# Kernel tuning notes

Hardware: AMD Instinct MI355X
Metric: run time of the kernel (lower is better)

## Reference

```python
import jax, jax.numpy as jnp
import numpy as np

B, T, D = 2, 2048, 1024
HEADS, UNITS = 16, 64
OUT_DIM = 1024
_LARGE_BIAS = 10000.0


def _uniform(key, shape, fan_in, fan_out):
    limit = np.sqrt(6.0 / (fan_in + fan_out))
    return jax.random.uniform(key, shape, jnp.float32, -limit, limit)


def setup_inputs() -> dict:
    key = jax.random.key(0)
    kx, kq, kk, kv, ko = jax.random.split(key, 5)
    x = jax.random.normal(kx, (B, T, D), jnp.float32)
    mask = jnp.ones((B, T), jnp.int32)
    Wq = _uniform(kq, (D, HEADS * UNITS), D, UNITS)
    Wk = _uniform(kk, (D, HEADS * UNITS), D, UNITS)
    Wv = _uniform(kv, (D, HEADS * UNITS), D, UNITS)
    Wo = _uniform(ko, (HEADS * UNITS, OUT_DIM), HEADS * UNITS, OUT_DIM)
    return {"x": x, "mask": mask, "Wq": Wq, "Wk": Wk, "Wv": Wv, "Wo": Wo}


def reference(x, mask, Wq, Wk, Wv, Wo):
    m = mask.astype(x.dtype)                      # [B, T]
    x = x * m[:, :, None]                         # zero padded positions
    b, t, _ = x.shape
    # projections, split heads: [B, T, H, U]
    q = (x @ Wq).reshape(b, t, HEADS, UNITS)
    k = (x @ Wk).reshape(b, t, HEADS, UNITS)
    v = (x @ Wv).reshape(b, t, HEADS, UNITS)
    # logits[b,h,i,j] = sum_u q[b,i,h,u] k[b,j,h,u]
    logits = jnp.einsum('bihu,bjhu->bhij', q, k) / np.sqrt(UNITS).astype(x.dtype)
    # causal (forward) mask: subtract large bias above the diagonal
    causal = jnp.triu(jnp.full((t, t), _LARGE_BIAS, x.dtype), k=1)
    logits = logits - causal
    # padding mask on key axis
    logits = logits - ((1.0 - m) * _LARGE_BIAS)[:, None, None, :]
    weights = jax.nn.softmax(logits, axis=-1)     # [B, H, T, T]
    attended = jnp.einsum('bhij,bjhu->bihu', weights, v)
    attended = attended.reshape(b, t, HEADS * UNITS)
    return attended @ Wo                          # [B, T, OUT_DIM]
```

## Files before the change

### kernel.cpp

```cpp
#include <hip/hip_runtime.h>
#include <stdint.h>
#include <stddef.h>

#define B_ 2
#define T_ 2048
#define D_ 1024
#define H_ 16
#define U_ 64
#define M_ (B_ * T_)
#define N_ (H_ * U_)

typedef __attribute__((ext_vector_type(4))) float f32x4;
typedef __attribute__((ext_vector_type(8))) short s16x8;
typedef __attribute__((ext_vector_type(8))) __bf16 b16x8;

static_assert(sizeof(s16x8) == 16, "frag size");

__device__ __forceinline__ unsigned short f2bf(float f) {
  unsigned int u = __float_as_uint(f);
  u += 0x7FFFu + ((u >> 16) & 1u);
  return (unsigned short)(u >> 16);
}

template <typename V>
__device__ __forceinline__ auto mfma16_impl(V a, V b, f32x4 c, int)
    -> decltype(__builtin_amdgcn_mfma_f32_16x16x32_bf16(a, b, c, 0, 0, 0)) {
  return __builtin_amdgcn_mfma_f32_16x16x32_bf16(a, b, c, 0, 0, 0);
}
template <typename V>
__device__ __forceinline__ f32x4 mfma16_impl(V a, V b, f32x4 c, long) {
  return __builtin_amdgcn_mfma_f32_16x16x32_bf16(
      __builtin_bit_cast(b16x8, a), __builtin_bit_cast(b16x8, b), c, 0, 0, 0);
}
__device__ __forceinline__ f32x4 mfma16(s16x8 a, s16x8 b, f32x4 c) {
  return mfma16_impl(a, b, c, 0);
}

__device__ __forceinline__ void gld16(const unsigned short* g, unsigned short* l) {
  __builtin_amdgcn_global_load_lds(
      (const __attribute__((address_space(1))) void*)g,
      (__attribute__((address_space(3))) void*)l, 16, 0, 0);
}

__global__ void wtrans_kernel(const float* __restrict__ w0, const float* __restrict__ w1,
                              const float* __restrict__ w2, const float* __restrict__ w3,
                              unsigned short* __restrict__ o0, unsigned short* __restrict__ o1,
                              unsigned short* __restrict__ o2, unsigned short* __restrict__ o3) {
  __shared__ float tile[64][65];
  const float* w;
  unsigned short* o;
  switch (blockIdx.z) {
    case 0: w = w0; o = o0; break;
    case 1: w = w1; o = o1; break;
    case 2: w = w2; o = o2; break;
    default: w = w3; o = o3; break;
  }
  const int kb = blockIdx.y * 64, nb = blockIdx.x * 64;
  const int tid = threadIdx.x;
  const int r0 = tid >> 6, c = tid & 63;
#pragma unroll
  for (int i = 0; i < 16; i++) {
    int r = i * 4 + r0;
    tile[r][c] = w[(size_t)(kb + r) * 1024 + nb + c];
  }
  __syncthreads();
#pragma unroll
  for (int i = 0; i < 16; i++) {
    int r = i * 4 + r0;
    o[(size_t)(nb + r) * 1024 + kb + c] = f2bf(tile[c][r]);
  }
}

__global__ void xmask_kernel(const float* __restrict__ x, const int* __restrict__ mask,
                             unsigned short* __restrict__ xb) {
  const int idx = (blockIdx.x * 256 + threadIdx.x) * 4;
  const int row = idx >> 10;
  const float m = (float)mask[row];
  float4 v = *(const float4*)(x + idx);
  ushort4 o;
  o.x = f2bf(v.x * m);
  o.y = f2bf(v.y * m);
  o.z = f2bf(v.z * m);
  o.w = f2bf(v.w * m);
  *(ushort4*)(xb + idx) = o;
}

template <int MODE>
__device__ __forceinline__ void gemm97_body(const unsigned short* __restrict__ A,
                                            const unsigned short* __restrict__ Bt,
                                            void* __restrict__ Cout) {
  constexpr int Kd = 1024, Nd = 1024;
  __shared__ unsigned short la[128 * 32];
  __shared__ unsigned short lb[128 * 32];
  const int tid = threadIdx.x;
  const int lane = tid & 63;
  const int w = tid >> 6;
  const int mb = blockIdx.y * 128, nb = blockIdx.x * 128;
  const int wm = (w >> 1) * 64, wn = (w & 1) * 64;
  const int lr = lane & 15, lg = lane >> 4;
  const int srow = w * 16 + (lane >> 2);
  const int scol = (lane & 3) * 8;
  const unsigned short* gA = A + (size_t)(mb + srow) * Kd + scol;
  const unsigned short* gB = Bt + (size_t)(nb + srow) * Kd + scol;
  unsigned short* lA = la + srow * 32 + scol;
  unsigned short* lB = lb + srow * 32 + scol;

  f32x4 acc[4][4] = {};

  for (int kt = 0; kt < Kd; kt += 32) {
    gld16(gA + kt, lA);
    gld16(gA + kt + (size_t)64 * Kd, lA + 64 * 32);
    gld16(gB + kt, lB);
    gld16(gB + kt + (size_t)64 * Kd, lB + 64 * 32);
    __syncthreads();
    s16x8 af[4], bfr[4];
#pragma unroll
    for (int i = 0; i < 4; i++)
      af[i] = *(const s16x8*)(la + (wm + i * 16 + lr) * 32 + lg * 8);
#pragma unroll
    for (int j = 0; j < 4; j++)
      bfr[j] = *(const s16x8*)(lb + (wn + j * 16 + lr) * 32 + lg * 8);
#pragma unroll
    for (int i = 0; i < 4; i++)
#pragma unroll
      for (int j = 0; j < 4; j++)
        acc[i][j] = mfma16(af[i], bfr[j], acc[i][j]);
    __syncthreads();
  }

#pragma unroll
  for (int i = 0; i < 4; i++)
#pragma unroll
    for (int j = 0; j < 4; j++) {
      const int col = nb + wn + j * 16 + lr;
      const int rowb = mb + wm + i * 16 + lg * 4;
      if (MODE == 1) {
        float* C = (float*)Cout;
#pragma unroll
        for (int r = 0; r < 4; r++) C[(size_t)(rowb + r) * Nd + col] = acc[i][j][r];
      } else if (MODE == 0) {
        unsigned short* C = (unsigned short*)Cout;
#pragma unroll
        for (int r = 0; r < 4; r++) C[(size_t)(rowb + r) * Nd + col] = f2bf(acc[i][j][r]);
      } else {
        unsigned short* C = (unsigned short*)Cout;
        const size_t vrow = ((size_t)(rowb >> 11) * 16 + (col >> 6)) * 64 + (col & 63);
        ushort4 o;
#pragma unroll
        for (int r = 0; r < 4; r++) ((unsigned short*)&o)[r] = f2bf(acc[i][j][r]);
        *(ushort4*)(C + vrow * T_ + (rowb & 2047)) = o;
      }
    }
}

__global__ __launch_bounds__(256) void gemm_qkv(const unsigned short* __restrict__ A,
                                                const unsigned short* __restrict__ wq,
                                                const unsigned short* __restrict__ wk,
                                                const unsigned short* __restrict__ wv,
                                                unsigned short* __restrict__ cq,
                                                unsigned short* __restrict__ ck,
                                                unsigned short* __restrict__ vt) {
  if (blockIdx.z == 0) {
    gemm97_body<0>(A, wq, cq);
  } else if (blockIdx.z == 1) {
    gemm97_body<0>(A, wk, ck);
  } else {
    gemm97_body<2>(A, wv, vt);
  }
}

__global__ __launch_bounds__(256) void gemm_out(const unsigned short* __restrict__ A,
                                                const unsigned short* __restrict__ woT,
                                                float* __restrict__ C) {
  gemm97_body<1>(A, woT, C);
}

__global__ __launch_bounds__(64) void attn12_kernel(const unsigned short* __restrict__ Q,
                                                    const unsigned short* __restrict__ K,
                                                    const unsigned short* __restrict__ Vt,
                                                    const int* __restrict__ mask,
                                                    unsigned short* __restrict__ att) {
  __shared__ unsigned short pbuf[32 * 64];
  const int lane = threadIdx.x & 63;
  const int li = lane & 15, lg = lane >> 4;
  const int bh = blockIdx.x & 31;
  const int b = bh >> 4, h = bh & 15;
  const int qg = 63 - (blockIdx.x >> 5);
  const int q0 = qg * 32;

  const float CS = 0.125f * 1.44269504089f;
  const float PB = 10000.0f * 1.44269504089f;
  const float THR = 8.0f;

  s16x8 qf[2][2];
#pragma unroll
  for (int f = 0; f < 2; f++) {
    const unsigned short* qrow = Q + ((size_t)(b * T_) + q0 + f * 16 + li) * 1024 + h * 64;
    qf[f][0] = *(const s16x8*)(qrow + lg * 8);
    qf[f][1] = *(const s16x8*)(qrow + 32 + lg * 8);
  }

  const unsigned short* Kb = K + (size_t)(b * T_) * 1024 + h * 64;
  const unsigned short* Vtb = Vt + (size_t)bh * 64 * T_;
  const int* mk = mask + b * T_;

  const int iq0 = q0 + li, iq1 = q0 + 16 + li;

  float mrun[2] = {-1e30f, -1e30f};
  float lpart[2] = {0.f, 0.f};
  f32x4 acc[4][2] = {};

  const int xr = (li & 3) << 5;
  char* pbb = (char*)pbuf;

  const int ntiles = (q0 + 95) >> 6;
  for (int t = 0; t < ntiles; t++) {
    const int jb = t * 64;
    const bool diag = (jb + 64 > q0);

    int4 mv[4];
#pragma unroll
    for (int jf = 0; jf < 4; jf++)
      mv[jf] = *(const int4*)(mk + jb + jf * 16 + lg * 4);

    f32x4 s[4][2] = {};
#pragma unroll
    for (int jf = 0; jf < 4; jf++) {
      const unsigned short* kr = Kb + (size_t)(jb + jf * 16 + li) * 1024 + lg * 8;
      s16x8 ka = *(const s16x8*)kr;
      s16x8 kc = *(const s16x8*)(kr + 32);
      s[jf][0] = mfma16(ka, qf[0][0], s[jf][0]);
      s[jf][0] = mfma16(kc, qf[0][1], s[jf][0]);
      s[jf][1] = mfma16(ka, qf[1][0], s[jf][1]);
      s[jf][1] = mfma16(kc, qf[1][1], s[jf][1]);
    }

    s16x8 vf[4][2];
#pragma unroll
    for (int uf = 0; uf < 4; uf++) {
      const unsigned short* vr = Vtb + (size_t)(uf * 16 + li) * T_ + jb + lg * 8;
      vf[uf][0] = *(const s16x8*)vr;
      vf[uf][1] = *(const s16x8*)(vr + 32);
    }

    float bias[4][4];
#pragma unroll
    for (int jf = 0; jf < 4; jf++) {
      bias[jf][0] = mv[jf].x ? 0.f : -PB;
      bias[jf][1] = mv[jf].y ? 0.f : -PB;
      bias[jf][2] = mv[jf].z ? 0.f : -PB;
      bias[jf][3] = mv[jf].w ? 0.f : -PB;
    }

#pragma unroll
    for (int f = 0; f < 2; f++) {
      const int iq = f ? iq1 : iq0;
      float pmax = -3e38f;
#pragma unroll
      for (int jf = 0; jf < 4; jf++) {
        f32x4 zz;
#pragma unroll
        for (int r = 0; r < 4; r++) {
          float z = fmaf(s[jf][f][r], CS, bias[jf][r]);
          if (diag && (jb + jf * 16 + lg * 4 + r > iq)) z = -1e30f;
          zz[r] = z;
          pmax = fmaxf(pmax, z);
        }
        s[jf][f] = zz;
      }
      if (!__all(pmax <= mrun[f] + THR)) {
        float rmax = fmaxf(pmax, __shfl_xor(pmax, 16));
        rmax = fmaxf(rmax, __shfl_xor(rmax, 32));
        const float mnew = fmaxf(mrun[f], rmax);
        const float al = exp2f(mrun[f] - mnew);
        lpart[f] *= al;
#pragma unroll
        for (int uf = 0; uf < 4; uf++) acc[uf][f] *= al;
        mrun[f] = mnew;
      }
      const float mm = mrun[f];
#pragma unroll
      for (int jf = 0; jf < 4; jf++) {
        ushort4 w4;
#pragma unroll
        for (int r = 0; r < 4; r++) {
          const float p = exp2f(s[jf][f][r] - mm);
          lpart[f] += p;
          ((unsigned short*)&w4)[r] = __builtin_bit_cast(unsigned short, (__bf16)p);
        }
        const int wb = (((f * 16 + li) * 64 + jf * 16 + lg * 4) * 2) ^ xr;
        *(ushort4*)(pbb + wb) = w4;
      }
    }

    s16x8 pfrag[2][2];
#pragma unroll
    for (int f = 0; f < 2; f++)
#pragma unroll
      for (int hh = 0; hh < 2; hh++) {
        const int rd = (((f * 16 + li) * 64 + hh * 32 + lg * 8) * 2) ^ xr;
        pfrag[f][hh] = *(const s16x8*)(pbb + rd);
      }
#pragma unroll
    for (int uf = 0; uf < 4; uf++)
#pragma unroll
      for (int f = 0; f < 2; f++) {
        acc[uf][f] = mfma16(vf[uf][0], pfrag[f][0], acc[uf][f]);
        acc[uf][f] = mfma16(vf[uf][1], pfrag[f][1], acc[uf][f]);
      }
  }

#pragma unroll
  for (int f = 0; f < 2; f++) {
    float l = lpart[f];
    l += __shfl_xor(l, 16);
    l += __shfl_xor(l, 32);
    const float inv = 1.0f / l;
    unsigned short* arow = att + ((size_t)(b * T_) + q0 + f * 16 + li) * 1024 + h * 64;
#pragma unroll
    for (int uf = 0; uf < 4; uf++) {
      ushort4 o;
#pragma unroll
      for (int r = 0; r < 4; r++)
        ((unsigned short*)&o)[r] = __builtin_bit_cast(unsigned short, (__bf16)(acc[uf][f][r] * inv));
      *(ushort4*)(arow + uf * 16 + lg * 4) = o;
    }
  }
}

extern "C" void kernel_launch(void* const* d_in, const int* in_sizes, int n_in,
                              void* d_out, int out_size, void* d_ws, size_t ws_size,
                              hipStream_t stream) {
  const float* x = (const float*)d_in[0];
  const int* mask = (const int*)d_in[1];
  const float* Wq = (const float*)d_in[2];
  const float* Wk = (const float*)d_in[3];
  const float* Wv = (const float*)d_in[4];
  const float* Wo = (const float*)d_in[5];

  const size_t MB = 1u << 20;
  char* ws = (char*)d_ws;
  unsigned short* wqT = (unsigned short*)(ws + 0 * MB);
  unsigned short* wkT = (unsigned short*)(ws + 2 * MB);
  unsigned short* wvT = (unsigned short*)(ws + 4 * MB);
  unsigned short* woT = (unsigned short*)(ws + 6 * MB);
  unsigned short* xb  = (unsigned short*)(ws + 8 * MB);
  unsigned short* qb  = (unsigned short*)(ws + 16 * MB);
  unsigned short* kb  = (unsigned short*)(ws + 24 * MB);
  unsigned short* vt  = (unsigned short*)(ws + 32 * MB);
  unsigned short* att = xb;
  (void)ws_size; (void)in_sizes; (void)n_in; (void)out_size;

  wtrans_kernel<<<dim3(16, 16, 4), 256, 0, stream>>>(Wq, Wk, Wv, Wo, wqT, wkT, wvT, woT);
  xmask_kernel<<<dim3(4096), 256, 0, stream>>>(x, mask, xb);
  gemm_qkv<<<dim3(8, 32, 3), 256, 0, stream>>>(xb, wqT, wkT, wvT, qb, kb, vt);
  attn12_kernel<<<dim3(2048), 64, 0, stream>>>(qb, kb, vt, mask, att);
  gemm_out<<<dim3(8, 32), 256, 0, stream>>>(att, woT, (float*)d_out);
}
```

Baseline: 154.1 us.

## Double-buffer K tile loads and add fast path for all-valid mask tiles

The attention loop now prefetches the next K tile into registers while the current one is used, ping-ponging between two register buffers through a lambda body unrolled by two. It also checks whether the whole mask tile is valid and, if so, skips the per-element padding bias select. The row-sum accumulation becomes a vector of four partial sums that are reduced at the end. The aim is to hide global-load latency for K and cut scalar ALU work in the softmax, at the cost of more registers per lane, which could reduce occupancy.

```diff
diff --git a/kernel.cpp b/kernel.cpp
--- a/kernel.cpp
+++ b/kernel.cpp
@@ -175,7 +175,7 @@
   gemm97_body<1>(A, woT, C);
 }
 
-__global__ __launch_bounds__(64) void attn12_kernel(const unsigned short* __restrict__ Q,
+__global__ __launch_bounds__(64) void attn13_kernel(const unsigned short* __restrict__ Q,
                                                     const unsigned short* __restrict__ K,
                                                     const unsigned short* __restrict__ Vt,
                                                     const int* __restrict__ mask,
@@ -207,14 +207,27 @@
   const int iq0 = q0 + li, iq1 = q0 + 16 + li;
 
   float mrun[2] = {-1e30f, -1e30f};
-  float lpart[2] = {0.f, 0.f};
+  f32x4 lp[2] = {};
   f32x4 acc[4][2] = {};
 
   const int xr = (li & 3) << 5;
   char* pbb = (char*)pbuf;
 
   const int ntiles = (q0 + 95) >> 6;
-  for (int t = 0; t < ntiles; t++) {
+
+  auto loadK = [&](s16x8 (&dst)[4][2], int jb) {
+#pragma unroll
+    for (int jf = 0; jf < 4; jf++) {
+      const unsigned short* kr = Kb + (size_t)(jb + jf * 16 + li) * 1024 + lg * 8;
+      dst[jf][0] = *(const s16x8*)kr;
+      dst[jf][1] = *(const s16x8*)(kr + 32);
+    }
+  };
+
+  s16x8 kA[4][2], kB[4][2];
+  loadK(kA, 0);
+
+  auto body = [&](int t, s16x8 (&kc)[4][2], s16x8 (&kn)[4][2]) {
     const int jb = t * 64;
     const bool diag = (jb + 64 > q0);
 
@@ -226,14 +239,13 @@
     f32x4 s[4][2] = {};
 #pragma unroll
     for (int jf = 0; jf < 4; jf++) {
-      const unsigned short* kr = Kb + (size_t)(jb + jf * 16 + li) * 1024 + lg * 8;
-      s16x8 ka = *(const s16x8*)kr;
-      s16x8 kc = *(const s16x8*)(kr + 32);
-      s[jf][0] = mfma16(ka, qf[0][0], s[jf][0]);
-      s[jf][0] = mfma16(kc, qf[0][1], s[jf][0]);
-      s[jf][1] = mfma16(ka, qf[1][0], s[jf][1]);
-      s[jf][1] = mfma16(kc, qf[1][1], s[jf][1]);
-    }
+      s[jf][0] = mfma16(kc[jf][0], qf[0][0], s[jf][0]);
+      s[jf][0] = mfma16(kc[jf][1], qf[0][1], s[jf][0]);
+      s[jf][1] = mfma16(kc[jf][0], qf[1][0], s[jf][1]);
+      s[jf][1] = mfma16(kc[jf][1], qf[1][1], s[jf][1]);
+    }
+
+    if (t + 1 < ntiles) loadK(kn, jb + 64);
 
     s16x8 vf[4][2];
 #pragma unroll
@@ -243,37 +255,49 @@
       vf[uf][1] = *(const s16x8*)(vr + 32);
     }
 
-    float bias[4][4];
-#pragma unroll
-    for (int jf = 0; jf < 4; jf++) {
-      bias[jf][0] = mv[jf].x ? 0.f : -PB;
-      bias[jf][1] = mv[jf].y ? 0.f : -PB;
-      bias[jf][2] = mv[jf].z ? 0.f : -PB;
-      bias[jf][3] = mv[jf].w ? 0.f : -PB;
-    }
+    const int band = (mv[0].x & mv[0].y & mv[0].z & mv[0].w) &
+                     (mv[1].x & mv[1].y & mv[1].z & mv[1].w) &
+                     (mv[2].x & mv[2].y & mv[2].z & mv[2].w) &
+                     (mv[3].x & mv[3].y & mv[3].z & mv[3].w);
+    const bool noBias = __all(band != 0);
 
 #pragma unroll
     for (int f = 0; f < 2; f++) {
       const int iq = f ? iq1 : iq0;
-      float pmax = -3e38f;
-#pragma unroll
-      for (int jf = 0; jf < 4; jf++) {
-        f32x4 zz;
-#pragma unroll
-        for (int r = 0; r < 4; r++) {
-          float z = fmaf(s[jf][f][r], CS, bias[jf][r]);
-          if (diag && (jb + jf * 16 + lg * 4 + r > iq)) z = -1e30f;
-          zz[r] = z;
-          pmax = fmaxf(pmax, z);
+      f32x4 pv = {-3e38f, -3e38f, -3e38f, -3e38f};
+      if (noBias) {
+#pragma unroll
+        for (int jf = 0; jf < 4; jf++) {
+          f32x4 zz = s[jf][f] * CS;
+          if (diag) {
+#pragma unroll
+            for (int r = 0; r < 4; r++)
+              if (jb + jf * 16 + lg * 4 + r > iq) zz[r] = -1e30f;
+          }
+          s[jf][f] = zz;
+          pv = __builtin_elementwise_max(pv, zz);
         }
-        s[jf][f] = zz;
-      }
+      } else {
+#pragma unroll
+        for (int jf = 0; jf < 4; jf++) {
+          f32x4 zz;
+#pragma unroll
+          for (int r = 0; r < 4; r++) {
+            float z = fmaf(s[jf][f][r], CS, ((&mv[jf].x)[r] ? 0.f : -PB));
+            if (diag && (jb + jf * 16 + lg * 4 + r > iq)) z = -1e30f;
+            zz[r] = z;
+          }
+          s[jf][f] = zz;
+          pv = __builtin_elementwise_max(pv, zz);
+        }
+      }
+      const float pmax = fmaxf(fmaxf(pv[0], pv[1]), fmaxf(pv[2], pv[3]));
       if (!__all(pmax <= mrun[f] + THR)) {
         float rmax = fmaxf(pmax, __shfl_xor(pmax, 16));
         rmax = fmaxf(rmax, __shfl_xor(rmax, 32));
         const float mnew = fmaxf(mrun[f], rmax);
         const float al = exp2f(mrun[f] - mnew);
-        lpart[f] *= al;
+        lp[f] *= al;
 #pragma unroll
         for (int uf = 0; uf < 4; uf++) acc[uf][f] *= al;
         mrun[f] = mnew;
@@ -281,13 +305,14 @@
       const float mm = mrun[f];
 #pragma unroll
       for (int jf = 0; jf < 4; jf++) {
+        f32x4 p;
+#pragma unroll
+        for (int r = 0; r < 4; r++) p[r] = exp2f(s[jf][f][r] - mm);
+        lp[f] += p;
         ushort4 w4;
 #pragma unroll
-        for (int r = 0; r < 4; r++) {
-          const float p = exp2f(s[jf][f][r] - mm);
-          lpart[f] += p;
-          ((unsigned short*)&w4)[r] = __builtin_bit_cast(unsigned short, (__bf16)p);
-        }
+        for (int r = 0; r < 4; r++)
+          ((unsigned short*)&w4)[r] = __builtin_bit_cast(unsigned short, (__bf16)p[r]);
         const int wb = (((f * 16 + li) * 64 + jf * 16 + lg * 4) * 2) ^ xr;
         *(ushort4*)(pbb + wb) = w4;
       }
@@ -308,11 +333,18 @@
         acc[uf][f] = mfma16(vf[uf][0], pfrag[f][0], acc[uf][f]);
         acc[uf][f] = mfma16(vf[uf][1], pfrag[f][1], acc[uf][f]);
       }
-  }
+  };
+
+  int t = 0;
+  for (; t + 1 < ntiles; t += 2) {
+    body(t, kA, kB);
+    body(t + 1, kB, kA);
+  }
+  if (t < ntiles) body(t, kA, kB);
 
 #pragma unroll
   for (int f = 0; f < 2; f++) {
-    float l = lpart[f];
+    float l = (lp[f][0] + lp[f][1]) + (lp[f][2] + lp[f][3]);
     l += __shfl_xor(l, 16);
     l += __shfl_xor(l, 32);
     const float inv = 1.0f / l;
@@ -354,6 +386,6 @@
   wtrans_kernel<<<dim3(16, 16, 4), 256, 0, stream>>>(Wq, Wk, Wv, Wo, wqT, wkT, wvT, woT);
   xmask_kernel<<<dim3(4096), 256, 0, stream>>>(x, mask, xb);
   gemm_qkv<<<dim3(8, 32, 3), 256, 0, stream>>>(xb, wqT, wkT, wvT, qb, kb, vt);
-  attn12_kernel<<<dim3(2048), 64, 0, stream>>>(qb, kb, vt, mask, att);
+  attn13_kernel<<<dim3(2048), 64, 0, stream>>>(qb, kb, vt, mask, att);
   gemm_out<<<dim3(8, 32), 256, 0, stream>>>(att, woT, (float*)d_out);
 }
```

After: 145.8 us. 1.06x faster.
